# Performance work log

Hardware: AMD Instinct MI355X
Metric: run time of the kernel (lower is better)

The kernel has to match this reference:

```python
import jax, jax.numpy as jnp
import numpy as np

EPS = 1e-5

def _ln(x, g, b):
    mu = jnp.mean(x, axis=-1, keepdims=True)
    var = jnp.var(x, axis=-1, keepdims=True)
    return (x - mu) * jax.lax.rsqrt(var + EPS) * g + b

def setup_inputs() -> dict:
    key = jax.random.key(0)
    ks = jax.random.split(key, 8)
    B, S, D, DK, DV = 8, 2048, 1024, 128, 128
    sD = 1.0 / np.sqrt(D)
    sDV = 1.0 / np.sqrt(DV)
    sH = 1.0 / np.sqrt(4 * D)
    return {
        "x": jax.random.normal(ks[0], (B, S, D), jnp.float32),
        "ln1_g": jnp.ones((D,), jnp.float32),
        "ln1_b": jnp.zeros((D,), jnp.float32),
        "Wq": jax.random.normal(ks[1], (D, DK), jnp.float32) * sD,
        "bq": jnp.zeros((DK,), jnp.float32),
        "Wk": jax.random.normal(ks[2], (D, DK), jnp.float32) * sD,
        "bk": jnp.zeros((DK,), jnp.float32),
        "Wv": jax.random.normal(ks[3], (D, DV), jnp.float32) * sD,
        "bv": jnp.zeros((DV,), jnp.float32),
        "Wo": jax.random.normal(ks[4], (DV, D), jnp.float32) * sDV,
        "bo": jnp.zeros((D,), jnp.float32),
        "ln2_g": jnp.ones((D,), jnp.float32),
        "ln2_b": jnp.zeros((D,), jnp.float32),
        "W1": jax.random.normal(ks[5], (D, 4 * D), jnp.float32) * sD,
        "b1": jnp.zeros((4 * D,), jnp.float32),
        "W2": jax.random.normal(ks[6], (4 * D, D), jnp.float32) * sH,
        "b2": jnp.zeros((D,), jnp.float32),
    }

def reference(x, ln1_g, ln1_b, Wq, bq, Wk, bk, Wv, bv, Wo, bo, ln2_g, ln2_b, W1, b1, W2, b2):
    # Block.forward (scaling_test=None): pre-LN, naive full attention, residual MLP
    xn = _ln(x, ln1_g, ln1_b)                       # [B,S,D]
    q = xn @ Wq + bq                                # [B,S,DK]
    k = xn @ Wk + bk                                # [B,S,DK]
    v = xn @ Wv + bv                                # [B,S,DV]
    scale = 1.0 / np.sqrt(q.shape[-1])
    S = jnp.einsum("bqd,bkd->bqk", q, k) * scale    # [B,S,S] materialized scores
    A = jax.nn.softmax(S, axis=-1)
    H = jnp.einsum("bqk,bkv->bqv", A, v)            # [B,S,DV]
    y = xn + (H @ Wo + bo)                          # note: residual uses ln1(x), as in source
    h = _ln(y, ln2_g, ln2_b)
    mlp = jax.nn.gelu(h @ W1 + b1, approximate=False) @ W2 + b2
    return y + mlp
```

## Files before the change

### kernel.cpp

```cpp
#include <hip/hip_runtime.h>
#include <math.h>

#define M_TOT   16384
#define D_MODEL 1024
#define D_HEAD  128
#define SEQ     2048
#define NBATCH  8
#define D_FF    4096

typedef _Float16 f16x8 __attribute__((ext_vector_type(8)));
typedef _Float16 f16x4 __attribute__((ext_vector_type(4)));
typedef float    f32x4 __attribute__((ext_vector_type(4)));

#define ATT_SCALE 0.08838834764831845f

__device__ __forceinline__ void gload_lds16(const _Float16* g, _Float16* l) {
  __builtin_amdgcn_global_load_lds(
      (const __attribute__((address_space(1))) unsigned int*)g,
      (__attribute__((address_space(3))) unsigned int*)l, 16, 0, 0);
}
__device__ __forceinline__ unsigned short f16bits(float v) {
  union { _Float16 f; unsigned short u; } cv; cv.f = (_Float16)v; return cv.u;
}
__device__ __forceinline__ float gelu_f(float x) {
  const float t = 0.7978845608028654f * x * (1.0f + 0.044715f * x * x);
  const float e = __expf(2.0f * t);
  const float th = 1.0f - 2.0f / (e + 1.0f);
  return 0.5f * x * (1.0f + th);
}

__global__ __launch_bounds__(256) void convt_kernel(const float* __restrict__ in,
                                                    _Float16* __restrict__ out,
                                                    int K, int N) {
  __shared__ float t[32][33];
  const int n0 = blockIdx.x * 32, k0 = blockIdx.y * 32;
  const int tx = threadIdx.x & 31, ty = threadIdx.x >> 5;
#pragma unroll
  for (int r = 0; r < 4; r++)
    t[ty + 8 * r][tx] = in[(size_t)(k0 + ty + 8 * r) * N + n0 + tx];
  __syncthreads();
#pragma unroll
  for (int r = 0; r < 4; r++)
    out[(size_t)(n0 + ty + 8 * r) * K + k0 + tx] = (_Float16)t[tx][ty + 8 * r];
}

template <bool WF32>
__global__ __launch_bounds__(256) void ln_kernel(const float* __restrict__ in,
                                                 const float* __restrict__ gamma,
                                                 const float* __restrict__ beta,
                                                 float* __restrict__ of,
                                                 _Float16* __restrict__ oh) {
  __shared__ float shs[4], shq[4];
  const int row = blockIdx.x;
  const int t = threadIdx.x;
  float4 v = ((const float4*)(in + (size_t)row * D_MODEL))[t];
  float s = v.x + v.y + v.z + v.w;
  float q = v.x * v.x + v.y * v.y + v.z * v.z + v.w * v.w;
#pragma unroll
  for (int o = 32; o > 0; o >>= 1) {
    s += __shfl_down(s, o, 64);
    q += __shfl_down(q, o, 64);
  }
  const int lane = t & 63, w = t >> 6;
  if (lane == 0) { shs[w] = s; shq[w] = q; }
  __syncthreads();
  if (t == 0) {
    shs[0] = shs[0] + shs[1] + shs[2] + shs[3];
    shq[0] = shq[0] + shq[1] + shq[2] + shq[3];
  }
  __syncthreads();
  const float mu = shs[0] * (1.0f / D_MODEL);
  const float var = shq[0] * (1.0f / D_MODEL) - mu * mu;
  const float rs = rsqrtf(var + 1e-5f);
  float4 gv = ((const float4*)gamma)[t];
  float4 bv = ((const float4*)beta)[t];
  float4 o;
  o.x = (v.x - mu) * rs * gv.x + bv.x;
  o.y = (v.y - mu) * rs * gv.y + bv.y;
  o.z = (v.z - mu) * rs * gv.z + bv.z;
  o.w = (v.w - mu) * rs * gv.w + bv.w;
  if (WF32) ((float4*)(of + (size_t)row * D_MODEL))[t] = o;
  f16x4 h4 = {(_Float16)o.x, (_Float16)o.y, (_Float16)o.z, (_Float16)o.w};
  ((f16x4*)(oh + (size_t)row * D_MODEL))[t] = h4;
}

template <int MODE>
__global__ __launch_bounds__(256) void mfma_gemm(const _Float16* __restrict__ A,
                                                 const _Float16* __restrict__ BT,
                                                 const float* __restrict__ b0p,
                                                 const float* __restrict__ b1p,
                                                 const float* __restrict__ b2p,
                                                 const float* __restrict__ res,
                                                 void* __restrict__ Cout,
                                                 _Float16* __restrict__ vtout,
                                                 int M, int N, int K) {
  __shared__ _Float16 SMEM[2 * 128 * 32];
  _Float16* As = SMEM;
  _Float16* Bs = SMEM + 128 * 32;
  const int tid = threadIdx.x;
  const int lane = tid & 63, w = tid >> 6;
  const int wr = w >> 1, wc = w & 1;
  const int row0 = blockIdx.y << 7, col0 = blockIdx.x << 7;
  const int l15 = lane & 15, quad = lane >> 4;
  const f32x4 zero = {0.f, 0.f, 0.f, 0.f};
  f32x4 acc[4][4];
#pragma unroll
  for (int i = 0; i < 4; i++)
#pragma unroll
    for (int j = 0; j < 4; j++) acc[i][j] = zero;

  const int srow = lane >> 2;
  const int scol = (lane & 3) << 3;
  const _Float16* Ag = A + (size_t)(row0 + w * 32 + srow) * K + scol;
  const _Float16* Bg = BT + (size_t)(col0 + w * 32 + srow) * K + scol;

  for (int k0 = 0; k0 < K; k0 += 32) {
#pragma unroll
    for (int p = 0; p < 2; p++) {
      gload_lds16(Ag + (size_t)(p * 16) * K + k0, &As[(w * 32 + p * 16) * 32]);
      gload_lds16(Bg + (size_t)(p * 16) * K + k0, &Bs[(w * 32 + p * 16) * 32]);
    }
    __syncthreads();
    f16x8 af[4], bfr[4];
#pragma unroll
    for (int i = 0; i < 4; i++) {
      af[i]  = *(const f16x8*)&As[(wr * 64 + i * 16 + l15) * 32 + quad * 8];
      bfr[i] = *(const f16x8*)&Bs[(wc * 64 + i * 16 + l15) * 32 + quad * 8];
    }
#pragma unroll
    for (int i = 0; i < 4; i++)
#pragma unroll
      for (int j = 0; j < 4; j++)
        acc[i][j] = __builtin_amdgcn_mfma_f32_16x16x32_f16(af[i], bfr[j], acc[i][j], 0, 0, 0);
    __syncthreads();
  }

  if (MODE == 0) {
    float* C = (float*)Cout;
    float bv4[4];
#pragma unroll
    for (int j = 0; j < 4; j++) bv4[j] = b0p[col0 + wc * 64 + j * 16 + l15];
#pragma unroll
    for (int i = 0; i < 4; i++)
#pragma unroll
      for (int r = 0; r < 4; r++) {
        const int row = row0 + wr * 64 + i * 16 + quad * 4 + r;
        const size_t base = (size_t)row * N + col0 + wc * 64 + l15;
        const float* rp = res + base;
        float* cp = C + base;
#pragma unroll
        for (int j = 0; j < 4; j++)
          cp[j * 16] = acc[i][j][r] + bv4[j] + rp[j * 16];
      }
  } else if (MODE == 1) {
    _Float16* C = (_Float16*)Cout;
    float bv4[4];
#pragma unroll
    for (int j = 0; j < 4; j++) bv4[j] = b0p[col0 + wc * 64 + j * 16 + l15];
#pragma unroll
    for (int i = 0; i < 4; i++)
#pragma unroll
      for (int r = 0; r < 4; r++) {
        const int row = row0 + wr * 64 + i * 16 + quad * 4 + r;
        _Float16* cp = C + (size_t)row * N + col0 + wc * 64 + l15;
#pragma unroll
        for (int j = 0; j < 4; j++)
          cp[j * 16] = (_Float16)gelu_f(acc[i][j][r] + bv4[j]);
      }
  } else {
    _Float16* qkout = (_Float16*)Cout;
    const int bx = blockIdx.x;
    if (bx < 2) {
      const float* bp = (bx == 0) ? b0p : b1p;
      const float sc = (bx == 0) ? ATT_SCALE : 1.0f;
      const int cofs = bx * 128 + wc * 64 + l15;
      float bv4[4];
#pragma unroll
      for (int j = 0; j < 4; j++) bv4[j] = bp[wc * 64 + j * 16 + l15];
#pragma unroll
      for (int i = 0; i < 4; i++)
#pragma unroll
        for (int r = 0; r < 4; r++) {
          const int row = row0 + wr * 64 + i * 16 + quad * 4 + r;
          _Float16* cp = qkout + (size_t)row * 256 + cofs;
#pragma unroll
          for (int j = 0; j < 4; j++)
            cp[j * 16] = (_Float16)((acc[i][j][r] + bv4[j]) * sc);
        }
    } else {
      _Float16* Ts = SMEM;
      float bv4[4];
#pragma unroll
      for (int j = 0; j < 4; j++) bv4[j] = b2p[wc * 64 + j * 16 + l15];
      const int bb = row0 >> 11, s0 = row0 & 2047;
#pragma unroll
      for (int c = 0; c < 4; c++) {
        __syncthreads();
        if (wr == (c >> 1)) {
#pragma unroll
          for (int ii = 0; ii < 2; ii++) {
            const int i = (c & 1) * 2 + ii;
#pragma unroll
            for (int j = 0; j < 4; j++) {
              const int vd = wc * 64 + j * 16 + l15;
              const int slocal = ii * 16 + quad * 4;
              ushort4 h;
              h.x = f16bits(acc[i][j][0] + bv4[j]);
              h.y = f16bits(acc[i][j][1] + bv4[j]);
              h.z = f16bits(acc[i][j][2] + bv4[j]);
              h.w = f16bits(acc[i][j][3] + bv4[j]);
              *(ushort4*)&Ts[vd * 40 + slocal] = h;
            }
          }
        }
        __syncthreads();
#pragma unroll
        for (int p = 0; p < 2; p++) {
          const int idx = tid + p * 256;
          const int vd = idx >> 2, s8 = (idx & 3) * 8;
          uint4 d = *(const uint4*)&Ts[vd * 40 + s8];
          *(uint4*)&vtout[((size_t)bb * 128 + vd) * SEQ + s0 + c * 32 + s8] = d;
        }
      }
    }
  }
}

__global__ __launch_bounds__(256) void flash_attn_mfma(const _Float16* __restrict__ qk,
                                                       const _Float16* __restrict__ vt,
                                                       _Float16* __restrict__ H) {
  __shared__ _Float16 Ks[2][64][136];
  __shared__ _Float16 Vs[128][72];
  __shared__ _Float16 Ps[4][16][72];
  const int b = blockIdx.y, q0 = blockIdx.x * 64;
  const int tid = threadIdx.x;
  const int lane = tid & 63, w = tid >> 6;
  const int l15 = lane & 15, quad = lane >> 4;

  f16x8 qf[4];
  {
    const _Float16* qrow = qk + ((size_t)(b * SEQ + q0 + w * 16 + l15)) * 256 + quad * 8;
#pragma unroll
    for (int ks = 0; ks < 4; ks++) qf[ks] = *(const f16x8*)(qrow + ks * 32);
  }
  const f32x4 zero = {0.f, 0.f, 0.f, 0.f};
  f32x4 O[8];
#pragma unroll
  for (int i = 0; i < 8; i++) O[i] = zero;
  float m_r[4] = {-1e30f, -1e30f, -1e30f, -1e30f};
  float l_r[4] = {0.f, 0.f, 0.f, 0.f};

  const _Float16* kg0 = qk + (size_t)(b * SEQ) * 256 + 128 + (size_t)(tid >> 4) * 256 + (tid & 15) * 8;
  const _Float16* vg0 = vt + (size_t)b * 128 * SEQ + (size_t)((tid >> 3)) * SEQ + (tid & 7) * 8;
  uint4 kp[4], vp[4];

#define LOAD_TILE(kt)                                                            \
  {                                                                              \
    const _Float16* kg = kg0 + (size_t)(kt) * 64 * 256;                          \
    const _Float16* vg = vg0 + (size_t)(kt) * 64;                                \
    _Pragma("unroll") for (int p = 0; p < 4; p++) {                              \
      kp[p] = *(const uint4*)(kg + (size_t)p * 16 * 256);                        \
      vp[p] = *(const uint4*)(vg + (size_t)p * 32 * SEQ);                        \
    }                                                                            \
  }
#define STORE_K(buf)                                                             \
  _Pragma("unroll") for (int p = 0; p < 4; p++)                                  \
      *(uint4*)&Ks[buf][(tid >> 4) + 16 * p][(tid & 15) * 8] = kp[p];
#define STORE_V()                                                                \
  _Pragma("unroll") for (int p = 0; p < 4; p++)                                  \
      *(uint4*)&Vs[(tid >> 3) + 32 * p][(tid & 7) * 8] = vp[p];

  LOAD_TILE(0);
  STORE_K(0);
  STORE_V();
  __syncthreads();

  const int NT = SEQ / 64;
  for (int kt = 0; kt < NT; kt++) {
    const int cur = kt & 1;
    if (kt + 1 < NT) LOAD_TILE(kt + 1);

    f32x4 s4[4];
#pragma unroll
    for (int nt = 0; nt < 4; nt++) {
      s4[nt] = zero;
#pragma unroll
      for (int ks = 0; ks < 4; ks++) {
        f16x8 kf = *(const f16x8*)&Ks[cur][nt * 16 + l15][ks * 32 + quad * 8];
        s4[nt] = __builtin_amdgcn_mfma_f32_16x16x32_f16(qf[ks], kf, s4[nt], 0, 0, 0);
      }
    }
    float rmax[4], alpha[4], rsum[4];
#pragma unroll
    for (int r = 0; r < 4; r++)
      rmax[r] = fmaxf(fmaxf(s4[0][r], s4[1][r]), fmaxf(s4[2][r], s4[3][r]));
#pragma unroll
    for (int o = 1; o < 16; o <<= 1)
#pragma unroll
      for (int r = 0; r < 4; r++) rmax[r] = fmaxf(rmax[r], __shfl_xor(rmax[r], o, 64));
#pragma unroll
    for (int r = 0; r < 4; r++) {
      const float nm = fmaxf(m_r[r], rmax[r]);
      alpha[r] = __expf(m_r[r] - nm);
      m_r[r] = nm;
#pragma unroll
      for (int nt = 0; nt < 4; nt++) s4[nt][r] = __expf(s4[nt][r] - nm);
      rsum[r] = s4[0][r] + s4[1][r] + s4[2][r] + s4[3][r];
    }
#pragma unroll
    for (int o = 1; o < 16; o <<= 1)
#pragma unroll
      for (int r = 0; r < 4; r++) rsum[r] += __shfl_xor(rsum[r], o, 64);
#pragma unroll
    for (int r = 0; r < 4; r++) {
      l_r[r] = l_r[r] * alpha[r] + rsum[r];
#pragma unroll
      for (int i = 0; i < 8; i++) O[i][r] *= alpha[r];
    }
#pragma unroll
    for (int nt = 0; nt < 4; nt++)
#pragma unroll
      for (int r = 0; r < 4; r++)
        Ps[w][quad * 4 + r][nt * 16 + l15] = (_Float16)s4[nt][r];
    f16x8 pa[2];
#pragma unroll
    for (int ks = 0; ks < 2; ks++)
      pa[ks] = *(const f16x8*)&Ps[w][l15][ks * 32 + quad * 8];
#pragma unroll
    for (int ks = 0; ks < 2; ks++)
#pragma unroll
      for (int vt8 = 0; vt8 < 8; vt8++) {
        f16x8 vf = *(const f16x8*)&Vs[vt8 * 16 + l15][ks * 32 + quad * 8];
        O[vt8] = __builtin_amdgcn_mfma_f32_16x16x32_f16(pa[ks], vf, O[vt8], 0, 0, 0);
      }

    if (kt + 1 < NT) {
      STORE_K(cur ^ 1);
      __syncthreads();
      STORE_V();
      __syncthreads();
    }
  }
#pragma unroll
  for (int r = 0; r < 4; r++) {
    const float inv = 1.0f / l_r[r];
    _Float16* hp = H + (size_t)(b * SEQ + q0 + w * 16 + quad * 4 + r) * D_HEAD;
#pragma unroll
    for (int vt8 = 0; vt8 < 8; vt8++)
      hp[vt8 * 16 + l15] = (_Float16)(O[vt8][r] * inv);
  }
}

extern "C" void kernel_launch(void* const* d_in, const int* in_sizes, int n_in,
                              void* d_out, int out_size, void* d_ws, size_t ws_size,
                              hipStream_t stream) {
  const float* x     = (const float*)d_in[0];
  const float* ln1_g = (const float*)d_in[1];
  const float* ln1_b = (const float*)d_in[2];
  const float* Wq    = (const float*)d_in[3];
  const float* bq    = (const float*)d_in[4];
  const float* Wk    = (const float*)d_in[5];
  const float* bk    = (const float*)d_in[6];
  const float* Wv    = (const float*)d_in[7];
  const float* bv    = (const float*)d_in[8];
  const float* Wo    = (const float*)d_in[9];
  const float* bo    = (const float*)d_in[10];
  const float* ln2_g = (const float*)d_in[11];
  const float* ln2_b = (const float*)d_in[12];
  const float* W1    = (const float*)d_in[13];
  const float* b1    = (const float*)d_in[14];
  const float* W2    = (const float*)d_in[15];
  const float* b2    = (const float*)d_in[16];
  float* out = (float*)d_out;

  char* ws = (char*)d_ws;
  const size_t MB = 1024 * 1024;
  _Float16* W1T   = (_Float16*)(ws);
  _Float16* W2T   = (_Float16*)(ws + 8 * MB);
  _Float16* WqkvT = (_Float16*)(ws + 16 * MB);
  _Float16* WoT   = (_Float16*)(ws + 16 * MB + 768 * 1024);
  float*    xn_f32 = (float*)(ws + 20 * MB);
  _Float16* xn_f16 = (_Float16*)(ws + 84 * MB);
  _Float16* qkb  = (_Float16*)(ws + 116 * MB);
  _Float16* vtb  = (_Float16*)(ws + 124 * MB);
  _Float16* Hb   = (_Float16*)(ws + 128 * MB);
  _Float16* act  = (_Float16*)(ws + 20 * MB);
  _Float16* h16  = (_Float16*)(ws + 148 * MB);

  convt_kernel<<<dim3(D_FF / 32, D_MODEL / 32), 256, 0, stream>>>(W1, W1T, D_MODEL, D_FF);
  convt_kernel<<<dim3(D_MODEL / 32, D_FF / 32), 256, 0, stream>>>(W2, W2T, D_FF, D_MODEL);
  convt_kernel<<<dim3(D_HEAD / 32, D_MODEL / 32), 256, 0, stream>>>(Wq, WqkvT, D_MODEL, D_HEAD);
  convt_kernel<<<dim3(D_HEAD / 32, D_MODEL / 32), 256, 0, stream>>>(Wk, WqkvT + 128 * 1024, D_MODEL, D_HEAD);
  convt_kernel<<<dim3(D_HEAD / 32, D_MODEL / 32), 256, 0, stream>>>(Wv, WqkvT + 256 * 1024, D_MODEL, D_HEAD);
  convt_kernel<<<dim3(D_MODEL / 32, D_HEAD / 32), 256, 0, stream>>>(Wo, WoT, D_HEAD, D_MODEL);
  ln_kernel<true><<<dim3(M_TOT), 256, 0, stream>>>(x, ln1_g, ln1_b, xn_f32, xn_f16);
  mfma_gemm<2><<<dim3(3, M_TOT / 128), 256, 0, stream>>>(
      xn_f16, WqkvT, bq, bk, bv, nullptr, qkb, vtb, M_TOT, 384, D_MODEL);
  flash_attn_mfma<<<dim3(SEQ / 64, NBATCH), 256, 0, stream>>>(qkb, vtb, Hb);
  mfma_gemm<0><<<dim3(D_MODEL / 128, M_TOT / 128), 256, 0, stream>>>(
      Hb, WoT, bo, nullptr, nullptr, xn_f32, out, nullptr, M_TOT, D_MODEL, D_HEAD);
  ln_kernel<false><<<dim3(M_TOT), 256, 0, stream>>>(out, ln2_g, ln2_b, nullptr, h16);
  mfma_gemm<1><<<dim3(D_FF / 128, M_TOT / 128), 256, 0, stream>>>(
      h16, W1T, b1, nullptr, nullptr, nullptr, act, nullptr, M_TOT, D_FF, D_MODEL);
  mfma_gemm<0><<<dim3(D_MODEL / 128, M_TOT / 128), 256, 0, stream>>>(
      act, W2T, b2, nullptr, nullptr, out, out, nullptr, M_TOT, D_MODEL, D_FF);

  (void)in_sizes; (void)n_in; (void)out_size; (void)ws_size;
}
```

Before: 796.8 us.

## Add 256x256-tile MFMA GEMM with 4-stage LDS pipeline for Wo and MLP

Introduces a new GEMM kernel with 256x256 output tiles, 512 threads, a 4-deep LDS ring buffer filled by direct global-to-LDS loads, XOR-swizzled LDS addressing and an XCD-aware block remap. The Wo projection and both MLP GEMMs now use it in place of the 128x128 kernel. The aim is more data reuse per loaded byte, more memory latency hidden, and fewer LDS bank conflicts in the large FFN GEMMs. The cost is much higher register and LDS pressure (128 KB LDS per block) and hand-placed waitcnt and barrier logic. The K=128 Wo GEMM gets only four k-tiles, so the pipeline barely fills there.

```diff
diff --git a/kernel.cpp b/kernel.cpp
--- a/kernel.cpp
+++ b/kernel.cpp
@@ -27,6 +27,15 @@
   const float e = __expf(2.0f * t);
   const float th = 1.0f - 2.0f / (e + 1.0f);
   return 0.5f * x * (1.0f + th);
+}
+__device__ __forceinline__ void bar_sync() {
+  __asm__ volatile("" ::: "memory");
+  __builtin_amdgcn_s_barrier();
+  __asm__ volatile("" ::: "memory");
+}
+__device__ __forceinline__ int swzb(int row, int quad) {
+  const int e = (((row & 1) << 2) | quad) ^ ((row >> 1) & 7);
+  return ((row >> 1) << 7) | (e << 4);
 }
 
 __global__ __launch_bounds__(256) void convt_kernel(const float* __restrict__ in,
@@ -82,6 +91,139 @@
   if (WF32) ((float4*)(of + (size_t)row * D_MODEL))[t] = o;
   f16x4 h4 = {(_Float16)o.x, (_Float16)o.y, (_Float16)o.z, (_Float16)o.w};
   ((f16x4*)(oh + (size_t)row * D_MODEL))[t] = h4;
+}
+
+
+#define STAGE_A(JT)                                                       \
+  {                                                                       \
+    _Float16* ps_ = SM + (((JT) & 3) * 16384) + ldsA;                     \
+    const size_t kp_ = (size_t)(JT) * 32;                                 \
+    gload_lds16(Ag0 + kp_, ps_);                                          \
+    gload_lds16(Ag0 + 16 * (size_t)K + kp_, ps_ + 512);                   \
+  }
+#define STAGE_B(JT)                                                       \
+  {                                                                       \
+    _Float16* ps_ = SM + (((JT) & 3) * 16384) + ldsB;                     \
+    const size_t kp_ = (size_t)(JT) * 32;                                 \
+    gload_lds16(Bg0 + kp_, ps_);                                          \
+    gload_lds16(Bg0 + 16 * (size_t)K + kp_, ps_ + 512);                   \
+  }
+
+#define KTILE(JT, WSTR, PF)                                                    \
+  {                                                                            \
+    _Float16* sb_ = SM + (((JT) & 3) * 16384);                                 \
+    const char* Ab_ = (const char*)sb_;                                        \
+    const char* Bb_ = (const char*)(sb_ + 8192);                               \
+    f16x8 af[8], bfr[4];                                                       \
+    _Pragma("unroll") for (int m = 0; m < 8; ++m)                              \
+        af[m] = *(const f16x8*)(Ab_ + swzb(wm * 128 + m * 16 + l15, quad));    \
+    bfr[0] = *(const f16x8*)(Bb_ + swzb(wn * 64 + l15, quad));                 \
+    bfr[1] = *(const f16x8*)(Bb_ + swzb(wn * 64 + 16 + l15, quad));            \
+    if (PF) { STAGE_A((JT) + 3); }                                             \
+    bar_sync();                                                                \
+    asm volatile("s_waitcnt lgkmcnt(0)" ::: "memory");                         \
+    __builtin_amdgcn_sched_barrier(0);                                         \
+    __builtin_amdgcn_s_setprio(1);                                             \
+    _Pragma("unroll") for (int m = 0; m < 8; ++m) {                            \
+      acc[m][0] = __builtin_amdgcn_mfma_f32_16x16x32_f16(af[m], bfr[0], acc[m][0], 0, 0, 0); \
+      acc[m][1] = __builtin_amdgcn_mfma_f32_16x16x32_f16(af[m], bfr[1], acc[m][1], 0, 0, 0); \
+    }                                                                          \
+    __builtin_amdgcn_s_setprio(0);                                             \
+    bar_sync();                                                                \
+    bfr[2] = *(const f16x8*)(Bb_ + swzb(wn * 64 + 32 + l15, quad));            \
+    bfr[3] = *(const f16x8*)(Bb_ + swzb(wn * 64 + 48 + l15, quad));            \
+    if (PF) { STAGE_B((JT) + 3); }                                             \
+    asm volatile("s_waitcnt " WSTR ::: "memory");                              \
+    bar_sync();                                                                \
+    asm volatile("s_waitcnt lgkmcnt(0)" ::: "memory");                         \
+    __builtin_amdgcn_sched_barrier(0);                                         \
+    __builtin_amdgcn_s_setprio(1);                                             \
+    _Pragma("unroll") for (int m = 0; m < 8; ++m) {                            \
+      acc[m][2] = __builtin_amdgcn_mfma_f32_16x16x32_f16(af[m], bfr[2], acc[m][2], 0, 0, 0); \
+      acc[m][3] = __builtin_amdgcn_mfma_f32_16x16x32_f16(af[m], bfr[3], acc[m][3], 0, 0, 0); \
+    }                                                                          \
+    __builtin_amdgcn_s_setprio(0);                                             \
+    bar_sync();                                                                \
+  }
+
+template <int MODE>
+__global__ __launch_bounds__(512, 2) void mfma_gemm256(
+    const _Float16* __restrict__ A, const _Float16* __restrict__ BT,
+    const float* __restrict__ bias, const float* __restrict__ res,
+    void* __restrict__ Cout, int M, int N, int K) {
+  __shared__ __attribute__((aligned(16))) _Float16 SM[4 * 16384];
+  const int tid = threadIdx.x;
+  const int lane = tid & 63, w = tid >> 6;
+  const int l15 = lane & 15, quad = lane >> 4;
+  const int wm = w >> 2, wn = w & 3;
+
+  const int nwg = gridDim.x;
+  const int bid = (blockIdx.x & 7) * (nwg >> 3) + (blockIdx.x >> 3);
+  const int nbx = N >> 8;
+  const int bx = bid % nbx, by = bid / nbx;
+  const int row0 = by << 8, col0 = bx << 8;
+
+  const int rp = lane >> 3;
+  const int el = (lane & 7) ^ rp;
+  const int lr = (rp << 1) | (el >> 2);
+  const int lc = (el & 3) << 3;
+  const _Float16* Ag0 = A + (size_t)(row0 + w * 32 + lr) * K + lc;
+  const _Float16* Bg0 = BT + (size_t)(col0 + w * 32 + lr) * K + lc;
+  const int ldsA = w * 1024;
+  const int ldsB = 8192 + w * 1024;
+
+  const f32x4 zero = {0.f, 0.f, 0.f, 0.f};
+  f32x4 acc[8][4];
+#pragma unroll
+  for (int m = 0; m < 8; ++m)
+#pragma unroll
+    for (int n = 0; n < 4; ++n) acc[m][n] = zero;
+
+  const int NKT = K >> 5;
+  for (int t = 0; t < 3; ++t) { STAGE_A(t); STAGE_B(t); }
+  asm volatile("s_waitcnt vmcnt(8)" ::: "memory");
+  bar_sync();
+
+  int j = 0;
+#pragma unroll 1
+  for (; j + 3 < NKT; ++j) { KTILE(j, "vmcnt(8)", 1); }
+  KTILE(j, "vmcnt(4)", 0); ++j;
+  KTILE(j, "vmcnt(0)", 0); ++j;
+  KTILE(j, "vmcnt(0)", 0);
+
+  const int colb = col0 + wn * 64 + l15;
+  if (MODE == 0) {
+    float* C = (float*)Cout;
+    float bv[4];
+#pragma unroll
+    for (int n = 0; n < 4; ++n) bv[n] = bias[colb + n * 16];
+#pragma unroll
+    for (int m = 0; m < 8; ++m)
+#pragma unroll
+      for (int r = 0; r < 4; ++r) {
+        const int row = row0 + wm * 128 + m * 16 + quad * 4 + r;
+        const size_t base = (size_t)row * N + colb;
+        const float* rp2 = res + base;
+        float* cp = C + base;
+#pragma unroll
+        for (int n = 0; n < 4; ++n) cp[n * 16] = acc[m][n][r] + bv[n] + rp2[n * 16];
+      }
+  } else {
+    _Float16* C = (_Float16*)Cout;
+    float bv[4];
+#pragma unroll
+    for (int n = 0; n < 4; ++n) bv[n] = bias[colb + n * 16];
+#pragma unroll
+    for (int m = 0; m < 8; ++m)
+#pragma unroll
+      for (int r = 0; r < 4; ++r) {
+        const int row = row0 + wm * 128 + m * 16 + quad * 4 + r;
+        _Float16* cp = C + (size_t)row * N + colb;
+#pragma unroll
+        for (int n = 0; n < 4; ++n) cp[n * 16] = (_Float16)gelu_f(acc[m][n][r] + bv[n]);
+      }
+  }
+  (void)M;
 }
 
 template <int MODE>
@@ -397,13 +539,13 @@
   mfma_gemm<2><<<dim3(3, M_TOT / 128), 256, 0, stream>>>(
       xn_f16, WqkvT, bq, bk, bv, nullptr, qkb, vtb, M_TOT, 384, D_MODEL);
   flash_attn_mfma<<<dim3(SEQ / 64, NBATCH), 256, 0, stream>>>(qkb, vtb, Hb);
-  mfma_gemm<0><<<dim3(D_MODEL / 128, M_TOT / 128), 256, 0, stream>>>(
-      Hb, WoT, bo, nullptr, nullptr, xn_f32, out, nullptr, M_TOT, D_MODEL, D_HEAD);
+  mfma_gemm256<0><<<dim3((D_MODEL / 256) * (M_TOT / 256)), 512, 0, stream>>>(
+      Hb, WoT, bo, xn_f32, out, M_TOT, D_MODEL, D_HEAD);
   ln_kernel<false><<<dim3(M_TOT), 256, 0, stream>>>(out, ln2_g, ln2_b, nullptr, h16);
-  mfma_gemm<1><<<dim3(D_FF / 128, M_TOT / 128), 256, 0, stream>>>(
-      h16, W1T, b1, nullptr, nullptr, nullptr, act, nullptr, M_TOT, D_FF, D_MODEL);
-  mfma_gemm<0><<<dim3(D_MODEL / 128, M_TOT / 128), 256, 0, stream>>>(
-      act, W2T, b2, nullptr, nullptr, out, out, nullptr, M_TOT, D_MODEL, D_FF);
+  mfma_gemm256<1><<<dim3((D_FF / 256) * (M_TOT / 256)), 512, 0, stream>>>(
+      h16, W1T, b1, nullptr, act, M_TOT, D_FF, D_MODEL);
+  mfma_gemm256<0><<<dim3((D_MODEL / 256) * (M_TOT / 256)), 512, 0, stream>>>(
+      act, W2T, b2, out, out, M_TOT, D_MODEL, D_FF);
 
   (void)in_sizes; (void)n_in; (void)out_size; (void)ws_size;
 }
```

New measurement: 663.8 us. 1.2x faster.
